# Performance work log

Measured on AMD Instinct MI355X. Metric: run time of the kernel, lower is better.

## Reference

```python
import jax, jax.numpy as jnp
import numpy as np

N_NODES = 50000
N_EDGES = 800000
FIN = 128
FQK = 128
FV = 128
H = 8


def setup_inputs() -> dict:
    key = jax.random.key(0)
    k1, k2, k3, k4, k5 = jax.random.split(key, 5)
    x = jax.random.normal(k1, (N_NODES, FIN), dtype=jnp.float32)
    # nn.Linear(Fin, 2*Fqk+Fv, bias=False): weight shape [Ftot, Fin]
    W = jax.random.normal(k2, (2 * FQK + FV, FIN), dtype=jnp.float32) / np.sqrt(FIN)
    # src must be sorted (scatter_* assume batch[-1]+1 segments)
    src = jnp.sort(jax.random.randint(k3, (N_EDGES,), 0, N_NODES))
    dest = jax.random.randint(k4, (N_EDGES,), 0, N_NODES)
    ei = jnp.stack([src, dest])
    batch = jnp.sort(jax.random.randint(k5, (N_NODES,), 0, 64))
    return {"x": x, "W": W, "batch": batch, "ei": ei}


def reference(x, W, batch, ei):
    n = x.shape[0]
    Fh = FQK // H    # 16
    Fhv = FV // H    # 16
    scaling = float(Fh) ** (-0.5)
    src, dest = ei[0], ei[1]

    qkv = x @ W.T                                   # [n, 2*Fqk+Fv]
    q = (qkv[:, :FQK] * scaling).reshape(n, H, Fh)
    k = qkv[:, FQK:2 * FQK].reshape(n, H, Fh)
    v = qkv[:, 2 * FQK:].reshape(n, H, Fhv)

    # per-edge attention scores, one per head: [E, H]
    aw = jnp.einsum('ehf,ehf->eh', q[src], k[dest])
    # faithful to original scatter_softmax: subtract GLOBAL per-head max
    aw = aw - aw.max(axis=0)
    ex = jnp.exp(aw)
    denom = jax.ops.segment_sum(ex, src, num_segments=n)[src]   # [E, H]
    a = ex / denom

    out = jax.ops.segment_sum(a[:, :, None] * v[dest], src, num_segments=n)  # [n, H, Fhv]
    return out.reshape(n, H * Fhv)
```

## Files before the change

### kernel.cpp

```cpp
#include <hip/hip_runtime.h>
#include <hip/hip_fp16.h>
#include <math.h>

#define FIN_ 128

typedef _Float16 half2v __attribute__((ext_vector_type(2)));
typedef _Float16 half8v __attribute__((ext_vector_type(8)));
typedef __attribute__((ext_vector_type(4))) float float4v;

__device__ __forceinline__ half2v u2h(unsigned u) {
    union { unsigned u; half2v h; } c; c.u = u; return c.h;
}

__global__ __launch_bounds__(256) void cvt_and_rowptr(const float* __restrict__ x,
                                                      const float* __restrict__ W,
                                                      _Float16* __restrict__ xh,
                                                      _Float16* __restrict__ wh,
                                                      const int* __restrict__ src,
                                                      int* __restrict__ rowptr,
                                                      int nx8, int nw8, int nE, int n) {
    int i = blockIdx.x * blockDim.x + threadIdx.x;
    if (i < nx8 + nw8) {
        const float* s;
        _Float16* d;
        float sc = 1.0f;
        if (i < nx8) { s = x + (size_t)i * 8; d = xh + (size_t)i * 8; }
        else {
            const int k = i - nx8;
            if ((k >> 4) < 128) sc = 0.25f;
            s = W + (size_t)k * 8; d = wh + (size_t)k * 8;
        }
        const float4 a = *(const float4*)s;
        const float4 b = *(const float4*)(s + 4);
        half8v r;
        r[0] = (_Float16)(a.x * sc); r[1] = (_Float16)(a.y * sc);
        r[2] = (_Float16)(a.z * sc); r[3] = (_Float16)(a.w * sc);
        r[4] = (_Float16)(b.x * sc); r[5] = (_Float16)(b.y * sc);
        r[6] = (_Float16)(b.z * sc); r[7] = (_Float16)(b.w * sc);
        *(half8v*)d = r;
    } else {
        const int j = i - (nx8 + nw8);
        if (j > n) return;
        int lo = 0, hi = nE;
        while (lo < hi) {
            int mid = (lo + hi) >> 1;
            if (src[mid] < j) lo = mid + 1; else hi = mid;
        }
        rowptr[j] = lo;
    }
}

__global__ __launch_bounds__(256) void gemm_qkv_mfma(const _Float16* __restrict__ xh,
                                                     const _Float16* __restrict__ wh,
                                                     _Float16* __restrict__ qb,
                                                     _Float16* __restrict__ kv,
                                                     int n) {
    __shared__ _Float16 T[128][136];
    const int row0 = blockIdx.x * 128;
    const int f0   = blockIdx.y * 128;
    const int t = threadIdx.x;
    const int lane = t & 63;
    const int wave = t >> 6;
    const int wr = wave >> 1, wc = wave & 1;
    const int l15 = lane & 15, kg = lane >> 4;

    float4v acc[4][4];
#pragma unroll
    for (int i = 0; i < 4; ++i)
#pragma unroll
        for (int j = 0; j < 4; ++j) acc[i][j] = (float4v)0.f;

    int nodeIdx[4];
#pragma unroll
    for (int ni = 0; ni < 4; ++ni) {
        const int nd = row0 + wc * 64 + ni * 16 + l15;
        nodeIdx[ni] = (nd < n) ? nd : 0;
    }
    const size_t fbase = (size_t)(f0 + wr * 64 + l15) * FIN_;

#pragma unroll
    for (int half = 0; half < 2; ++half) {
#pragma unroll
        for (int ks = 0; ks < 2; ++ks) {
            const int koff = half * 64 + ks * 32 + kg * 8;
            half8v a[4], b[4];
#pragma unroll
            for (int mi = 0; mi < 4; ++mi)
                a[mi] = *(const half8v*)(wh + fbase + (size_t)mi * 16 * FIN_ + koff);
#pragma unroll
            for (int ni = 0; ni < 4; ++ni)
                b[ni] = *(const half8v*)(xh + (size_t)nodeIdx[ni] * FIN_ + koff);
#pragma unroll
            for (int mi = 0; mi < 4; ++mi)
#pragma unroll
                for (int ni = 0; ni < 4; ++ni)
                    acc[mi][ni] = __builtin_amdgcn_mfma_f32_16x16x32_f16(
                        a[mi], b[ni], acc[mi][ni], 0, 0, 0);
        }
    }

#pragma unroll
    for (int mi = 0; mi < 4; ++mi) {
        const int fb = wr * 64 + mi * 16 + kg * 4;
#pragma unroll
        for (int ni = 0; ni < 4; ++ni) {
            const int nl = wc * 64 + ni * 16 + l15;
            union { ushort4 u; _Float16 f[4]; } pk;
#pragma unroll
            for (int r = 0; r < 4; ++r) pk.f[r] = (_Float16)acc[mi][ni][r];
            *(ushort4*)&T[nl][fb] = pk.u;
        }
    }
    __syncthreads();
    const bool isq = (f0 == 0);
#pragma unroll
    for (int i = 0; i < 8; ++i) {
        const int u = t + i * 256;
        const int nl = u >> 4;
        const int cs = (u & 15) * 8;
        const int ng = row0 + nl;
        if (ng >= n) continue;
        const half8v val = *(const half8v*)&T[nl][cs];
        if (isq) *(half8v*)&qb[(size_t)ng * 128 + cs] = val;
        else     *(half8v*)&kv[(size_t)ng * 256 + (f0 - 128) + cs] = val;
    }
}

__device__ __forceinline__ float dot16(uint4 k0, uint4 k1, const half2v* q) {
#if __has_builtin(__builtin_amdgcn_fdot2)
    float s = __builtin_amdgcn_fdot2(u2h(k0.x), q[0], 0.f, false);
    s = __builtin_amdgcn_fdot2(u2h(k0.y), q[1], s, false);
    s = __builtin_amdgcn_fdot2(u2h(k0.z), q[2], s, false);
    s = __builtin_amdgcn_fdot2(u2h(k0.w), q[3], s, false);
    s = __builtin_amdgcn_fdot2(u2h(k1.x), q[4], s, false);
    s = __builtin_amdgcn_fdot2(u2h(k1.y), q[5], s, false);
    s = __builtin_amdgcn_fdot2(u2h(k1.z), q[6], s, false);
    s = __builtin_amdgcn_fdot2(u2h(k1.w), q[7], s, false);
    return s;
#else
    half2v a = u2h(k0.x) * q[0];
    a += u2h(k0.y) * q[1];
    a += u2h(k0.z) * q[2];
    a += u2h(k0.w) * q[3];
    a += u2h(k1.x) * q[4];
    a += u2h(k1.y) * q[5];
    a += u2h(k1.z) * q[6];
    a += u2h(k1.w) * q[7];
    return (float)a[0] + (float)a[1];
#endif
}

__global__ __launch_bounds__(256) void attn_edges_ep(const _Float16* __restrict__ qb,
                                                     const _Float16* __restrict__ kv,
                                                     const int* __restrict__ rowptr,
                                                     const int* __restrict__ dest,
                                                     float* __restrict__ out, int n) {
    const int wave = threadIdx.x >> 6;
    const int node = blockIdx.x * 4 + wave;
    if (node >= n) return;
    const int lane = threadIdx.x & 63;
    const int j = lane >> 3;
    const int h = lane & 7;
    const int ppos = ((j & 1) << 3) | ((j & 2) << 1) | ((j & 4) >> 1);
    float* outp = &out[(size_t)node * FIN_ + h * 16 + ppos];

    const int e0 = rowptr[node];
    const int e1 = rowptr[node + 1];
    if (e0 == e1) {
        *(float2*)outp = make_float2(0.f, 0.f);
        return;
    }

    half2v qh[8];
    {
        const uint4 q0 = *(const uint4*)(qb + (size_t)node * 128 + h * 16);
        const uint4 q1 = *(const uint4*)(qb + (size_t)node * 128 + h * 16 + 8);
        qh[0] = u2h(q0.x); qh[1] = u2h(q0.y); qh[2] = u2h(q0.z); qh[3] = u2h(q0.w);
        qh[4] = u2h(q1.x); qh[5] = u2h(q1.y); qh[6] = u2h(q1.z); qh[7] = u2h(q1.w);
    }

    float lsum = 0.f;
    half2v a8[8];
#pragma unroll
    for (int i = 0; i < 8; ++i) a8[i] = (half2v)(_Float16)0;

    const int hoff = h << 4;
    for (int eb = e0; eb < e1; eb += 16) {
        const int eA = eb + j;
        const int eB = eb + 8 + j;
        const bool vA = eA < e1;
        const bool vB = eB < e1;
        const unsigned dA = (unsigned)dest[vA ? eA : (e1 - 1)];
        const unsigned dB = (unsigned)dest[vB ? eB : (e1 - 1)];
        const unsigned offA = (dA << 8) + hoff;
        const unsigned offB = (dB << 8) + hoff;
        const uint4 k0A = *(const uint4*)(kv + offA);
        const uint4 k1A = *(const uint4*)(kv + offA + 8);
        const uint4 v0A = *(const uint4*)(kv + offA + 128);
        const uint4 v1A = *(const uint4*)(kv + offA + 136);
        const uint4 k0B = *(const uint4*)(kv + offB);
        const uint4 k1B = *(const uint4*)(kv + offB + 8);
        const uint4 v0B = *(const uint4*)(kv + offB + 128);
        const uint4 v1B = *(const uint4*)(kv + offB + 136);

        const float sA = dot16(k0A, k1A, qh);
        const float sB = dot16(k0B, k1B, qh);
        const float pA = vA ? __expf(sA) : 0.f;
        const float pB = vB ? __expf(sB) : 0.f;
        lsum += pA + pB;

        const _Float16 ha = (_Float16)pA, hb = (_Float16)pB;
        const half2v pa = {ha, ha}, pb = {hb, hb};
        a8[0] += pa * u2h(v0A.x) + pb * u2h(v0B.x);
        a8[1] += pa * u2h(v0A.y) + pb * u2h(v0B.y);
        a8[2] += pa * u2h(v0A.z) + pb * u2h(v0B.z);
        a8[3] += pa * u2h(v0A.w) + pb * u2h(v0B.w);
        a8[4] += pa * u2h(v1A.x) + pb * u2h(v1B.x);
        a8[5] += pa * u2h(v1A.y) + pb * u2h(v1B.y);
        a8[6] += pa * u2h(v1A.z) + pb * u2h(v1B.z);
        a8[7] += pa * u2h(v1A.w) + pb * u2h(v1B.w);
    }

    lsum += __shfl_xor(lsum, 8);
    lsum += __shfl_xor(lsum, 16);
    lsum += __shfl_xor(lsum, 32);

    float a16[16];
#pragma unroll
    for (int i = 0; i < 8; ++i) {
        a16[2 * i]     = (float)a8[i][0];
        a16[2 * i + 1] = (float)a8[i][1];
    }

    float r8[8];
    {
        const bool b = (j & 1) != 0;
#pragma unroll
        for (int i = 0; i < 8; ++i) {
            const float keep = b ? a16[i + 8] : a16[i];
            const float send = b ? a16[i] : a16[i + 8];
            r8[i] = keep + __shfl_xor(send, 8);
        }
    }
    float r4[4];
    {
        const bool b = (j & 2) != 0;
#pragma unroll
        for (int i = 0; i < 4; ++i) {
            const float keep = b ? r8[i + 4] : r8[i];
            const float send = b ? r8[i] : r8[i + 4];
            r4[i] = keep + __shfl_xor(send, 16);
        }
    }
    float r2[2];
    {
        const bool b = (j & 4) != 0;
#pragma unroll
        for (int i = 0; i < 2; ++i) {
            const float keep = b ? r4[i + 2] : r4[i];
            const float send = b ? r4[i] : r4[i + 2];
            r2[i] = keep + __shfl_xor(send, 32);
        }
    }

    const float inv = (lsum > 0.f) ? 1.f / lsum : 0.f;
    *(float2*)outp = make_float2(r2[0] * inv, r2[1] * inv);
}

extern "C" void kernel_launch(void* const* d_in, const int* in_sizes, int n_in,
                              void* d_out, int out_size, void* d_ws, size_t ws_size,
                              hipStream_t stream) {
    const float* x = (const float*)d_in[0];
    const float* W = (const float*)d_in[1];
    const int* ei = (const int*)d_in[3];

    const int n = in_sizes[0] / FIN_;
    const int nW = in_sizes[1];
    const int nE = in_sizes[3] / 2;
    const int* src = ei;
    const int* dest = ei + nE;

    char* w = (char*)d_ws;
    _Float16* qb = (_Float16*)w;   w += (size_t)n * 128 * 2;
    _Float16* kv = (_Float16*)w;   w += (size_t)n * 256 * 2;
    int* rowptr = (int*)w;         w += ((size_t)(n + 1) * 4 + 15) & ~(size_t)15;
    _Float16* xh = (_Float16*)w;   w += (size_t)n * FIN_ * 2;
    _Float16* wh = (_Float16*)w;
    float* out = (float*)d_out;

    const int nx8 = n * FIN_ / 8, nw8 = nW / 8;
    const int tot = nx8 + nw8 + n + 1;
    cvt_and_rowptr<<<(tot + 255) / 256, 256, 0, stream>>>(x, W, xh, wh, src, rowptr,
                                                          nx8, nw8, nE, n);

    dim3 g1((n + 127) / 128, 3);
    gemm_qkv_mfma<<<g1, 256, 0, stream>>>(xh, wh, qb, kv, n);

    attn_edges_ep<<<(n + 3) / 4, 256, 0, stream>>>(qb, kv, rowptr, dest, out, n);
}
```

Measured before the change: 96.32 us.

## Shrink QKV GEMM tiles to 64 rows and reorder rowptr blocks first

The QKV projection GEMM now uses 64-node by 128-feature tiles, with each wave owning 32 features. It runs on a flat 1D grid where the three feature slices of one node tile sit in adjacent blocks, so they share the x rows in cache. The conversion kernel now puts the rowptr binary-search threads first, padded to a whole block, so those latency-bound blocks start early and do not mix with the conversion threads. The smaller tiles double the block count and raise occupancy, but each x load feeds fewer MFMAs.

```diff
diff --git a/kernel.cpp b/kernel.cpp
--- a/kernel.cpp
+++ b/kernel.cpp
@@ -18,36 +18,38 @@
                                                       _Float16* __restrict__ wh,
                                                       const int* __restrict__ src,
                                                       int* __restrict__ rowptr,
-                                                      int nx8, int nw8, int nE, int n) {
-    int i = blockIdx.x * blockDim.x + threadIdx.x;
-    if (i < nx8 + nw8) {
-        const float* s;
-        _Float16* d;
-        float sc = 1.0f;
-        if (i < nx8) { s = x + (size_t)i * 8; d = xh + (size_t)i * 8; }
-        else {
-            const int k = i - nx8;
-            if ((k >> 4) < 128) sc = 0.25f;
-            s = W + (size_t)k * 8; d = wh + (size_t)k * 8;
-        }
-        const float4 a = *(const float4*)s;
-        const float4 b = *(const float4*)(s + 4);
-        half8v r;
-        r[0] = (_Float16)(a.x * sc); r[1] = (_Float16)(a.y * sc);
-        r[2] = (_Float16)(a.z * sc); r[3] = (_Float16)(a.w * sc);
-        r[4] = (_Float16)(b.x * sc); r[5] = (_Float16)(b.y * sc);
-        r[6] = (_Float16)(b.z * sc); r[7] = (_Float16)(b.w * sc);
-        *(half8v*)d = r;
-    } else {
-        const int j = i - (nx8 + nw8);
-        if (j > n) return;
+                                                      int nx8, int nw8, int nE, int n,
+                                                      int nrp) {
+    const int i = blockIdx.x * blockDim.x + threadIdx.x;
+    if (i < nrp) {
+        if (i > n) return;
         int lo = 0, hi = nE;
         while (lo < hi) {
             int mid = (lo + hi) >> 1;
-            if (src[mid] < j) lo = mid + 1; else hi = mid;
-        }
-        rowptr[j] = lo;
-    }
+            if (src[mid] < i) lo = mid + 1; else hi = mid;
+        }
+        rowptr[i] = lo;
+        return;
+    }
+    const int e = i - nrp;
+    if (e >= nx8 + nw8) return;
+    const float* s;
+    _Float16* d;
+    float sc = 1.0f;
+    if (e < nx8) { s = x + (size_t)e * 8; d = xh + (size_t)e * 8; }
+    else {
+        const int k = e - nx8;
+        if ((k >> 4) < 128) sc = 0.25f;
+        s = W + (size_t)k * 8; d = wh + (size_t)k * 8;
+    }
+    const float4 a = *(const float4*)s;
+    const float4 b = *(const float4*)(s + 4);
+    half8v r;
+    r[0] = (_Float16)(a.x * sc); r[1] = (_Float16)(a.y * sc);
+    r[2] = (_Float16)(a.z * sc); r[3] = (_Float16)(a.w * sc);
+    r[4] = (_Float16)(b.x * sc); r[5] = (_Float16)(b.y * sc);
+    r[6] = (_Float16)(b.z * sc); r[7] = (_Float16)(b.w * sc);
+    *(half8v*)d = r;
 }
 
 __global__ __launch_bounds__(256) void gemm_qkv_mfma(const _Float16* __restrict__ xh,
@@ -55,56 +57,54 @@
                                                      _Float16* __restrict__ qb,
                                                      _Float16* __restrict__ kv,
                                                      int n) {
-    __shared__ _Float16 T[128][136];
-    const int row0 = blockIdx.x * 128;
-    const int f0   = blockIdx.y * 128;
+    __shared__ _Float16 T[64][136];
+    const int bid = blockIdx.x;
+    const int bx = bid / 3, fsel = bid % 3;
+    const int row0 = bx * 64;
+    const int f0 = fsel * 128;
     const int t = threadIdx.x;
     const int lane = t & 63;
-    const int wave = t >> 6;
-    const int wr = wave >> 1, wc = wave & 1;
+    const int w = t >> 6;
     const int l15 = lane & 15, kg = lane >> 4;
 
-    float4v acc[4][4];
-#pragma unroll
-    for (int i = 0; i < 4; ++i)
+    float4v acc[2][4];
+#pragma unroll
+    for (int i = 0; i < 2; ++i)
 #pragma unroll
         for (int j = 0; j < 4; ++j) acc[i][j] = (float4v)0.f;
 
     int nodeIdx[4];
 #pragma unroll
     for (int ni = 0; ni < 4; ++ni) {
-        const int nd = row0 + wc * 64 + ni * 16 + l15;
+        const int nd = row0 + ni * 16 + l15;
         nodeIdx[ni] = (nd < n) ? nd : 0;
     }
-    const size_t fbase = (size_t)(f0 + wr * 64 + l15) * FIN_;
-
-#pragma unroll
-    for (int half = 0; half < 2; ++half) {
-#pragma unroll
-        for (int ks = 0; ks < 2; ++ks) {
-            const int koff = half * 64 + ks * 32 + kg * 8;
-            half8v a[4], b[4];
-#pragma unroll
-            for (int mi = 0; mi < 4; ++mi)
-                a[mi] = *(const half8v*)(wh + fbase + (size_t)mi * 16 * FIN_ + koff);
+    const size_t fbase = (size_t)(f0 + w * 32 + l15) * FIN_;
+
+#pragma unroll
+    for (int ks = 0; ks < 4; ++ks) {
+        const int koff = ks * 32 + kg * 8;
+        half8v a[2], b[4];
+#pragma unroll
+        for (int mi = 0; mi < 2; ++mi)
+            a[mi] = *(const half8v*)(wh + fbase + (size_t)mi * 16 * FIN_ + koff);
+#pragma unroll
+        for (int ni = 0; ni < 4; ++ni)
+            b[ni] = *(const half8v*)(xh + (size_t)nodeIdx[ni] * FIN_ + koff);
+#pragma unroll
+        for (int mi = 0; mi < 2; ++mi)
 #pragma unroll
             for (int ni = 0; ni < 4; ++ni)
-                b[ni] = *(const half8v*)(xh + (size_t)nodeIdx[ni] * FIN_ + koff);
-#pragma unroll
-            for (int mi = 0; mi < 4; ++mi)
-#pragma unroll
-                for (int ni = 0; ni < 4; ++ni)
-                    acc[mi][ni] = __builtin_amdgcn_mfma_f32_16x16x32_f16(
-                        a[mi], b[ni], acc[mi][ni], 0, 0, 0);
-        }
-    }
-
-#pragma unroll
-    for (int mi = 0; mi < 4; ++mi) {
-        const int fb = wr * 64 + mi * 16 + kg * 4;
+                acc[mi][ni] = __builtin_amdgcn_mfma_f32_16x16x32_f16(
+                    a[mi], b[ni], acc[mi][ni], 0, 0, 0);
+    }
+
+#pragma unroll
+    for (int mi = 0; mi < 2; ++mi) {
+        const int fb = w * 32 + mi * 16 + kg * 4;
 #pragma unroll
         for (int ni = 0; ni < 4; ++ni) {
-            const int nl = wc * 64 + ni * 16 + l15;
+            const int nl = ni * 16 + l15;
             union { ushort4 u; _Float16 f[4]; } pk;
 #pragma unroll
             for (int r = 0; r < 4; ++r) pk.f[r] = (_Float16)acc[mi][ni][r];
@@ -112,17 +112,18 @@
         }
     }
     __syncthreads();
-    const bool isq = (f0 == 0);
-#pragma unroll
-    for (int i = 0; i < 8; ++i) {
+    const bool isq = (fsel == 0);
+#pragma unroll
+    for (int i = 0; i < 4; ++i) {
         const int u = t + i * 256;
         const int nl = u >> 4;
         const int cs = (u & 15) * 8;
         const int ng = row0 + nl;
-        if (ng >= n) continue;
-        const half8v val = *(const half8v*)&T[nl][cs];
-        if (isq) *(half8v*)&qb[(size_t)ng * 128 + cs] = val;
-        else     *(half8v*)&kv[(size_t)ng * 256 + (f0 - 128) + cs] = val;
+        if (ng < n) {
+            const half8v val = *(const half8v*)&T[nl][cs];
+            if (isq) *(half8v*)&qb[(size_t)ng * 128 + cs] = val;
+            else     *(half8v*)&kv[(size_t)ng * 256 + (f0 - 128) + cs] = val;
+        }
     }
 }
 
@@ -289,12 +290,13 @@
     float* out = (float*)d_out;
 
     const int nx8 = n * FIN_ / 8, nw8 = nW / 8;
-    const int tot = nx8 + nw8 + n + 1;
+    const int nrp = ((n + 1 + 255) / 256) * 256;
+    const int tot = nrp + nx8 + nw8;
     cvt_and_rowptr<<<(tot + 255) / 256, 256, 0, stream>>>(x, W, xh, wh, src, rowptr,
-                                                          nx8, nw8, nE, n);
-
-    dim3 g1((n + 127) / 128, 3);
-    gemm_qkv_mfma<<<g1, 256, 0, stream>>>(xh, wh, qb, kv, n);
+                                                          nx8, nw8, nE, n, nrp);
+
+    const int nxb = (n + 63) / 64;
+    gemm_qkv_mfma<<<3 * nxb, 256, 0, stream>>>(xh, wh, qb, kv, n);
 
     attn_edges_ep<<<(n + 3) / 4, 256, 0, stream>>>(qb, kv, rowptr, dest, out, n);
 }
```

Measured after the change: 101.6 us. 5.5% more time.
